# Performance work log

Hardware: AMD Instinct MI355X
Metric: run time of the kernel (lower is better)

Reference implementation:

```python
import jax, jax.numpy as jnp
import numpy as np

B, T, C = 2, 2048, 768
H = 12
D = C // H  # head size = 64
F = 4 * C
EPS = 1e-5


def _layernorm(x, g, b):
    mu = jnp.mean(x, axis=-1, keepdims=True)
    var = jnp.var(x, axis=-1, keepdims=True)
    return (x - mu) * jax.lax.rsqrt(var + EPS) * g + b


def setup_inputs() -> dict:
    key = jax.random.key(0)
    ks = jax.random.split(key, 16)
    s_in = 1.0 / np.sqrt(C)
    s_ff = 1.0 / np.sqrt(F)
    return {
        "x": jax.random.normal(ks[0], (B, T, C), dtype=jnp.float32),
        # per-head projection weights, stacked [H, C, D] (no bias, as in nn.Linear(bias=False))
        "Wq": jax.random.uniform(ks[1], (H, C, D), jnp.float32, -s_in, s_in),
        "Wk": jax.random.uniform(ks[2], (H, C, D), jnp.float32, -s_in, s_in),
        "Wv": jax.random.uniform(ks[3], (H, C, D), jnp.float32, -s_in, s_in),
        "Wp": jax.random.uniform(ks[4], (C, C), jnp.float32, -s_in, s_in),
        "bp": jax.random.uniform(ks[5], (C,), jnp.float32, -s_in, s_in),
        "W1": jax.random.uniform(ks[6], (C, F), jnp.float32, -s_in, s_in),
        "b1": jax.random.uniform(ks[7], (F,), jnp.float32, -s_in, s_in),
        "W2": jax.random.uniform(ks[8], (F, C), jnp.float32, -s_ff, s_ff),
        "b2": jax.random.uniform(ks[9], (C,), jnp.float32, -s_ff, s_ff),
        "ln1_g": jnp.ones((C,), jnp.float32),
        "ln1_b": jnp.zeros((C,), jnp.float32),
        "ln2_g": jnp.ones((C,), jnp.float32),
        "ln2_b": jnp.zeros((C,), jnp.float32),
    }


def reference(x, Wq, Wk, Wv, Wp, bp, W1, b1, W2, b2, ln1_g, ln1_b, ln2_g, ln2_b):
    # --- self-attention sublayer (pre-LN) ---
    h = _layernorm(x, ln1_g, ln1_b)                      # [B,T,C]
    q = jnp.einsum('btc,hcd->bhtd', h, Wq)
    k = jnp.einsum('btc,hcd->bhtd', h, Wk)
    v = jnp.einsum('btc,hcd->bhtd', h, Wv)
    # NOTE: original scales by C**-0.5 where C = n_embd (full width), not head size
    scale = C ** (-0.5)
    wei = jnp.einsum('bhtd,bhsd->bhts', q, k) * scale    # [B,H,T,T]
    causal = jnp.tril(jnp.ones((T, T), dtype=bool))
    wei = jnp.where(causal, wei, -jnp.inf)
    wei = jax.nn.softmax(wei, axis=-1)
    out = jnp.einsum('bhts,bhsd->bhtd', wei, v)          # [B,H,T,D]
    out = out.transpose(0, 2, 1, 3).reshape(B, T, C)     # concat heads
    sa = out @ Wp + bp
    x = x + sa
    # --- feed-forward sublayer (pre-LN); ReLU after BOTH linears, as in source ---
    h2 = _layernorm(x, ln2_g, ln2_b)
    ff = jax.nn.relu(jax.nn.relu(h2 @ W1 + b1) @ W2 + b2)
    return x + ff
```

## Files before the change

### kernel.cpp

```cpp
#include <hip/hip_runtime.h>
#include <hip/hip_bf16.h>

#define TSEQ 2048
#define CDIM 768
#define NHEAD 12
#define DHEAD 64
#define FDIM 3072
#define MROWS 4096
#define BH 24

typedef __attribute__((ext_vector_type(8))) short short8;
typedef __attribute__((ext_vector_type(4))) float f32x4;

__device__ inline unsigned short f2bf(float f) {
  __hip_bfloat16 h = __float2bfloat16(f);
  return __builtin_bit_cast(unsigned short, h);
}

__device__ inline void gload16(const unsigned short* g, unsigned short* l) {
  __builtin_amdgcn_global_load_lds(
      (const __attribute__((address_space(1))) unsigned int*)g,
      (__attribute__((address_space(3))) unsigned int*)l, 16, 0, 0);
}

__global__ __launch_bounds__(256) void prep_all(
    const float* __restrict__ Wq, const float* __restrict__ Wk,
    const float* __restrict__ Wv, const float* __restrict__ Wp,
    const float* __restrict__ W1, const float* __restrict__ W2,
    unsigned short* __restrict__ WqkvT, unsigned short* __restrict__ WpT,
    unsigned short* __restrict__ W1T, unsigned short* __restrict__ W2T,
    const float* __restrict__ x, const float* __restrict__ ln1g,
    const float* __restrict__ ln1b, unsigned short* __restrict__ h1) {
  __shared__ float tile[32][33];
  __shared__ float red[8];
  int b = blockIdx.x;
  if (b >= 6912) {
    int row = b - 6912;
    int tid = threadIdx.x;
    const float* xr = x + (size_t)row * CDIM;
    float v[3];
    float s = 0.f;
#pragma unroll
    for (int i = 0; i < 3; ++i) { v[i] = xr[tid + i * 256]; s += v[i]; }
#pragma unroll
    for (int m = 1; m < 64; m <<= 1) s += __shfl_xor(s, m);
    int w = tid >> 6;
    if ((tid & 63) == 0) red[w] = s;
    __syncthreads();
    float mean = (red[0] + red[1] + red[2] + red[3]) * (1.f / CDIM);
    float vs = 0.f;
#pragma unroll
    for (int i = 0; i < 3; ++i) { float d = v[i] - mean; vs += d * d; }
#pragma unroll
    for (int m = 1; m < 64; m <<= 1) vs += __shfl_xor(vs, m);
    if ((tid & 63) == 0) red[4 + w] = vs;
    __syncthreads();
    float var = (red[4] + red[5] + red[6] + red[7]) * (1.f / CDIM);
    float rstd = rsqrtf(var + 1e-5f);
    unsigned short* orow = h1 + (size_t)row * CDIM;
#pragma unroll
    for (int i = 0; i < 3; ++i) {
      int c = tid + i * 256;
      orow[c] = f2bf((v[i] - mean) * rstd * ln1g[c] + ln1b[c]);
    }
    return;
  }
  int xx = threadIdx.x & 31, y = threadIdx.x >> 5;
  if (b < 1728) {
    int cx = b % 24, dy = (b / 24) % 2, ph = b / 48;
    int proj = ph / NHEAD, h = ph % NHEAD;
    const float* in = (proj == 0 ? Wq : (proj == 1 ? Wk : Wv)) + (size_t)h * CDIM * DHEAD;
    int c0 = cx * 32, d0 = dy * 32;
#pragma unroll
    for (int i = 0; i < 4; ++i)
      tile[y + i * 8][xx] = in[(size_t)(c0 + y + i * 8) * DHEAD + d0 + xx];
    __syncthreads();
#pragma unroll
    for (int i = 0; i < 4; ++i)
      WqkvT[(size_t)(proj * CDIM + h * DHEAD + d0 + y + i * 8) * CDIM + c0 + xx] =
          f2bf(tile[xx][y + i * 8]);
  } else {
    const float* in;
    unsigned short* out;
    int R, C, bx, by;
    if (b < 2304) {
      int b2 = b - 1728;
      in = Wp; out = WpT; R = CDIM; C = CDIM; bx = b2 % 24; by = b2 / 24;
    } else if (b < 4608) {
      int b2 = b - 2304;
      in = W1; out = W1T; R = CDIM; C = FDIM; bx = b2 % 96; by = b2 / 96;
    } else {
      int b2 = b - 4608;
      in = W2; out = W2T; R = FDIM; C = CDIM; bx = b2 % 24; by = b2 / 24;
    }
    int c0 = bx * 32, r0 = by * 32;
#pragma unroll
    for (int i = 0; i < 4; ++i)
      tile[y + i * 8][xx] = in[(size_t)(r0 + y + i * 8) * C + c0 + xx];
    __syncthreads();
#pragma unroll
    for (int i = 0; i < 4; ++i)
      out[(size_t)(c0 + y + i * 8) * R + r0 + xx] = f2bf(tile[xx][y + i * 8]);
  }
}

__global__ __launch_bounds__(256) void ln_kernel(
    const float* __restrict__ x, const float* __restrict__ g,
    const float* __restrict__ b, unsigned short* __restrict__ out) {
  int row = blockIdx.x;
  int tid = threadIdx.x;
  const float* xr = x + (size_t)row * CDIM;
  float v[3];
  float s = 0.f;
#pragma unroll
  for (int i = 0; i < 3; ++i) { v[i] = xr[tid + i * 256]; s += v[i]; }
#pragma unroll
  for (int m = 1; m < 64; m <<= 1) s += __shfl_xor(s, m);
  __shared__ float red[8];
  int w = tid >> 6;
  if ((tid & 63) == 0) red[w] = s;
  __syncthreads();
  float mean = (red[0] + red[1] + red[2] + red[3]) * (1.f / CDIM);
  float vs = 0.f;
#pragma unroll
  for (int i = 0; i < 3; ++i) { float d = v[i] - mean; vs += d * d; }
#pragma unroll
  for (int m = 1; m < 64; m <<= 1) vs += __shfl_xor(vs, m);
  if ((tid & 63) == 0) red[4 + w] = vs;
  __syncthreads();
  float var = (red[4] + red[5] + red[6] + red[7]) * (1.f / CDIM);
  float rstd = rsqrtf(var + 1e-5f);
  unsigned short* orow = out + (size_t)row * CDIM;
#pragma unroll
  for (int i = 0; i < 3; ++i) {
    int c = tid + i * 256;
    orow[c] = f2bf((v[i] - mean) * rstd * g[c] + b[c]);
  }
}

template <int EPI>
__global__ __launch_bounds__(256) void gemm_bt(
    const unsigned short* __restrict__ A, const unsigned short* __restrict__ BT,
    int M, int N, int K,
    const float* __restrict__ bias, const float* __restrict__ aux,
    float* __restrict__ outf, unsigned short* __restrict__ outb,
    unsigned short* __restrict__ qo, unsigned short* __restrict__ ko,
    unsigned short* __restrict__ vo) {
  __shared__ unsigned short As[3][128 * 64];
  __shared__ unsigned short Bs[3][64 * 64];
  int tid = threadIdx.x;
  int lane = tid & 63, wave = tid >> 6;
  int l15 = lane & 15, lg = lane >> 4;
  int lr = lane >> 3, lc = lane & 7;
  size_t bm = (size_t)blockIdx.x * 128, bn = (size_t)blockIdx.y * 64;
  f32x4 acc[2][4] = {};
  int nk = K >> 6;

  auto stage = [&](int tk, int buf) {
    int kt = tk * 64;
#pragma unroll
    for (int i = 0; i < 4; ++i) {
      int r0 = (wave * 4 + i) * 8;
      gload16(A + (bm + r0 + lr) * K + kt + (lc ^ lr) * 8, &As[buf][r0 * 64]);
    }
#pragma unroll
    for (int i = 0; i < 2; ++i) {
      int r0 = (wave * 2 + i) * 8;
      gload16(BT + (bn + r0 + lr) * K + kt + (lc ^ lr) * 8, &Bs[buf][r0 * 64]);
    }
  };

  stage(0, 0);
  if (nk > 1) {
    stage(1, 1);
    asm volatile("s_waitcnt vmcnt(6)" ::: "memory");
  } else {
    asm volatile("s_waitcnt vmcnt(0)" ::: "memory");
  }
  __builtin_amdgcn_s_barrier();

  int cur = 0;
  for (int tk = 0; tk < nk; ++tk) {
    bool pre = (tk + 2 < nk);
    if (pre) stage(tk + 2, (cur + 2 >= 3) ? cur - 1 : cur + 2);
    __builtin_amdgcn_s_setprio(1);
#pragma unroll
    for (int kk = 0; kk < 64; kk += 32) {
      int kb = kk + lg * 8;
      short8 af[2], bfr[4];
#pragma unroll
      for (int m = 0; m < 2; ++m) {
        int row = wave * 32 + m * 16 + l15;
        af[m] = *reinterpret_cast<const short8*>(&As[cur][row * 64 + (kb ^ ((row & 7) << 3))]);
      }
#pragma unroll
      for (int n = 0; n < 4; ++n) {
        int row = n * 16 + l15;
        bfr[n] = *reinterpret_cast<const short8*>(&Bs[cur][row * 64 + (kb ^ ((row & 7) << 3))]);
      }
#pragma unroll
      for (int m = 0; m < 2; ++m)
#pragma unroll
        for (int n = 0; n < 4; ++n)
          acc[m][n] = __builtin_amdgcn_mfma_f32_16x16x32_bf16(af[m], bfr[n], acc[m][n], 0, 0, 0);
    }
    __builtin_amdgcn_s_setprio(0);
    if (pre) asm volatile("s_waitcnt vmcnt(6)" ::: "memory");
    else     asm volatile("s_waitcnt vmcnt(0)" ::: "memory");
    __builtin_amdgcn_s_barrier();
    cur = (cur == 2) ? 0 : cur + 1;
  }

#pragma unroll
  for (int m = 0; m < 2; ++m) {
#pragma unroll
    for (int n = 0; n < 4; ++n) {
#pragma unroll
      for (int r = 0; r < 4; ++r) {
        int row = (int)bm + wave * 32 + m * 16 + lg * 4 + r;
        int col = (int)bn + n * 16 + l15;
        float val = acc[m][n][r];
        if constexpr (EPI == 0) {
          int proj = col / CDIM, rem = col % CDIM;
          int h = rem >> 6, d = rem & 63;
          int b = row >> 11, t = row & (TSEQ - 1);
          if (proj == 0) {
            qo[(((size_t)(b * NHEAD + h)) * TSEQ + t) * DHEAD + d] =
                f2bf(val * 0.05205877247186126f);
          } else if (proj == 1) {
            ko[(((size_t)(b * NHEAD + h)) * TSEQ + t) * DHEAD + d] = f2bf(val);
          } else {
            vo[(((size_t)(b * NHEAD + h)) * DHEAD + d) * TSEQ + t] = f2bf(val);
          }
        } else if constexpr (EPI == 1) {
          size_t idx = (size_t)row * CDIM + col;
          outf[idx] = val + bias[col] + aux[idx];
        } else if constexpr (EPI == 2) {
          size_t idx = (size_t)row * FDIM + col;
          outb[idx] = f2bf(fmaxf(val + bias[col], 0.f));
        } else {
          size_t idx = (size_t)row * CDIM + col;
          outf[idx] = aux[idx] + fmaxf(val + bias[col], 0.f);
        }
      }
    }
  }
}

__global__ __launch_bounds__(256) void attn_kernel(
    const unsigned short* __restrict__ Q, const unsigned short* __restrict__ Kd,
    const unsigned short* __restrict__ VT, unsigned short* __restrict__ O) {
  __shared__ unsigned short Kl[3][64 * 64];
  __shared__ unsigned short Vl[3][64 * 64];
  __shared__ unsigned short plds[4][16 * 64];
  int tid = threadIdx.x;
  int wave = tid >> 6, lane = tid & 63;
  int l15 = lane & 15, lg = lane >> 4;
  int bid = blockIdx.x;
  int xcd = bid & 7, idx = bid >> 3;
  int bh = xcd * 3 + idx / 16;
  int p = idx & 15;
  const unsigned short* qp = Q + (size_t)bh * TSEQ * DHEAD;
  const unsigned short* kp = Kd + (size_t)bh * TSEQ * DHEAD;
  const unsigned short* vp = VT + (size_t)bh * DHEAD * TSEQ;
  unsigned short* pw = plds[wave];
  int b = bh / NHEAD, h = bh % NHEAD;

  short8 ones;
  {
    unsigned short ov = (l15 == 0) ? (unsigned short)0x3F80 : (unsigned short)0;
#pragma unroll
    for (int j = 0; j < 8; ++j) ones[j] = (short)ov;
  }

  int lr = lane >> 3, lc = lane & 7;
  int jsw = lc ^ lr;

  auto stage = [&](int t, int buf) {
    int s0 = t * 64;
#pragma unroll
    for (int i = 0; i < 2; ++i) {
      int r0 = (wave * 2 + i) * 8;
      gload16(kp + (size_t)(s0 + r0 + lr) * DHEAD + jsw * 8, &Kl[buf][r0 * 64]);
      gload16(vp + (size_t)(r0 + lr) * TSEQ + s0 + jsw * 8, &Vl[buf][r0 * 64]);
    }
  };

  auto run_stripe = [&](int stripe) {
    int qbase = stripe * 64 + wave * 16;
    int nt = stripe + 1;
    short8 qf[2];
#pragma unroll
    for (int kk = 0; kk < 2; ++kk)
      qf[kk] = *reinterpret_cast<const short8*>(
          qp + (size_t)(qbase + l15) * DHEAD + kk * 32 + lg * 8);
    f32x4 oacc[5] = {};

    stage(0, 0);
    if (nt > 1) {
      stage(1, 1);
      asm volatile("s_waitcnt vmcnt(4)" ::: "memory");
    } else {
      asm volatile("s_waitcnt vmcnt(0)" ::: "memory");
    }
    __builtin_amdgcn_s_barrier();

    for (int t = 0; t < nt; ++t) {
      int cur = t % 3;
      bool pre2 = (t + 2 < nt);
      if (pre2) stage(t + 2, (t + 2) % 3);
      int s0 = t * 64;
      f32x4 sacc[4] = {};
      __builtin_amdgcn_s_setprio(1);
#pragma unroll
      for (int st = 0; st < 4; ++st) {
        int row = st * 16 + l15;
        int sw = row & 7;
#pragma unroll
        for (int kk = 0; kk < 2; ++kk) {
          short8 kf = *reinterpret_cast<const short8*>(
              &Kl[cur][row * 64 + (((kk * 4 + lg) ^ sw) * 8)]);
          sacc[st] = __builtin_amdgcn_mfma_f32_16x16x32_bf16(qf[kk], kf, sacc[st], 0, 0, 0);
        }
      }
      __builtin_amdgcn_s_setprio(0);
      bool last = (t == nt - 1);
#pragma unroll
      for (int r = 0; r < 4; ++r) {
        int qrow = qbase + lg * 4 + r;
        int prow = lg * 4 + r;
        int psw = (prow & 7) << 3;
        if (last) {
#pragma unroll
          for (int st = 0; st < 4; ++st) {
            float pv = exp2f(sacc[st][r]);
            if (s0 + st * 16 + l15 > qrow) pv = 0.f;
            pw[prow * 64 + ((st * 16 + l15) ^ psw)] = f2bf(pv);
          }
        } else {
#pragma unroll
          for (int st = 0; st < 4; ++st)
            pw[prow * 64 + ((st * 16 + l15) ^ psw)] = f2bf(exp2f(sacc[st][r]));
        }
      }
      int prsw = (l15 & 7) << 3;
      short8 pa0 = *reinterpret_cast<const short8*>(&pw[l15 * 64 + ((lg * 8) ^ prsw)]);
      short8 pa1 = *reinterpret_cast<const short8*>(&pw[l15 * 64 + ((32 + lg * 8) ^ prsw)]);
      __builtin_amdgcn_s_setprio(1);
#pragma unroll
      for (int n = 0; n < 4; ++n) {
        int row = n * 16 + l15;
        int sw = row & 7;
        short8 vf0 = *reinterpret_cast<const short8*>(&Vl[cur][row * 64 + ((lg ^ sw) * 8)]);
        oacc[n] = __builtin_amdgcn_mfma_f32_16x16x32_bf16(pa0, vf0, oacc[n], 0, 0, 0);
        short8 vf1 = *reinterpret_cast<const short8*>(&Vl[cur][row * 64 + (((4 + lg) ^ sw) * 8)]);
        oacc[n] = __builtin_amdgcn_mfma_f32_16x16x32_bf16(pa1, vf1, oacc[n], 0, 0, 0);
      }
      oacc[4] = __builtin_amdgcn_mfma_f32_16x16x32_bf16(pa0, ones, oacc[4], 0, 0, 0);
      oacc[4] = __builtin_amdgcn_mfma_f32_16x16x32_bf16(pa1, ones, oacc[4], 0, 0, 0);
      __builtin_amdgcn_s_setprio(0);
      if (pre2) asm volatile("s_waitcnt vmcnt(4)" ::: "memory");
      else      asm volatile("s_waitcnt vmcnt(0)" ::: "memory");
      __builtin_amdgcn_s_barrier();
    }

#pragma unroll
    for (int r = 0; r < 4; ++r) {
      float lsum = __shfl(oacc[4][r], lane & 48);
      float inv = 1.f / lsum;
      int row = qbase + lg * 4 + r;
#pragma unroll
      for (int n = 0; n < 4; ++n)
        O[(size_t)(b * TSEQ + row) * CDIM + h * DHEAD + n * 16 + l15] =
            f2bf(oacc[n][r] * inv);
    }
  };

  run_stripe(31 - p);
  run_stripe(p);
}

extern "C" void kernel_launch(void* const* d_in, const int* in_sizes, int n_in,
                              void* d_out, int out_size, void* d_ws, size_t ws_size,
                              hipStream_t stream) {
  const float* x    = (const float*)d_in[0];
  const float* Wq   = (const float*)d_in[1];
  const float* Wk   = (const float*)d_in[2];
  const float* Wv   = (const float*)d_in[3];
  const float* Wp   = (const float*)d_in[4];
  const float* bp   = (const float*)d_in[5];
  const float* W1   = (const float*)d_in[6];
  const float* b1   = (const float*)d_in[7];
  const float* W2   = (const float*)d_in[8];
  const float* b2   = (const float*)d_in[9];
  const float* ln1g = (const float*)d_in[10];
  const float* ln1b = (const float*)d_in[11];
  const float* ln2g = (const float*)d_in[12];
  const float* ln2b = (const float*)d_in[13];
  float* out = (float*)d_out;

  char* ws = (char*)d_ws;
  auto alloc = [&](size_t bytes) {
    char* p = ws;
    ws += (bytes + 255) & ~(size_t)255;
    return p;
  };
  unsigned short* h1    = (unsigned short*)alloc((size_t)MROWS * CDIM * 2);
  unsigned short* WqkvT = (unsigned short*)alloc((size_t)3 * CDIM * CDIM * 2);
  unsigned short* WpT   = (unsigned short*)alloc((size_t)CDIM * CDIM * 2);
  unsigned short* W1T   = (unsigned short*)alloc((size_t)FDIM * CDIM * 2);
  unsigned short* W2T   = (unsigned short*)alloc((size_t)CDIM * FDIM * 2);
  unsigned short* Qb    = (unsigned short*)alloc((size_t)BH * TSEQ * DHEAD * 2);
  unsigned short* Kb    = (unsigned short*)alloc((size_t)BH * TSEQ * DHEAD * 2);
  unsigned short* VTb   = (unsigned short*)alloc((size_t)BH * TSEQ * DHEAD * 2);
  unsigned short* AO    = (unsigned short*)alloc((size_t)MROWS * CDIM * 2);
  float*          x1    = (float*)alloc((size_t)MROWS * CDIM * 4);
  unsigned short* h2    = (unsigned short*)alloc((size_t)MROWS * CDIM * 2);
  unsigned short* a1    = (unsigned short*)alloc((size_t)MROWS * FDIM * 2);

  prep_all<<<11008, 256, 0, stream>>>(Wq, Wk, Wv, Wp, W1, W2,
                                      WqkvT, WpT, W1T, W2T, x, ln1g, ln1b, h1);
  gemm_bt<0><<<dim3(32, 36), 256, 0, stream>>>(h1, WqkvT, MROWS, 3 * CDIM, CDIM,
                                               nullptr, nullptr, nullptr, nullptr, Qb, Kb, VTb);
  attn_kernel<<<384, 256, 0, stream>>>(Qb, Kb, VTb, AO);
  gemm_bt<1><<<dim3(32, 12), 256, 0, stream>>>(AO, WpT, MROWS, CDIM, CDIM,
                                               bp, x, x1, nullptr, nullptr, nullptr, nullptr);
  ln_kernel<<<4096, 256, 0, stream>>>(x1, ln2g, ln2b, h2);
  gemm_bt<2><<<dim3(32, 48), 256, 0, stream>>>(h2, W1T, MROWS, FDIM, CDIM,
                                               b1, nullptr, nullptr, a1, nullptr, nullptr, nullptr);
  gemm_bt<3><<<dim3(32, 12), 256, 0, stream>>>(a1, W2T, MROWS, CDIM, FDIM,
                                               b2, x1, out, nullptr, nullptr, nullptr, nullptr);
}
```

Measured before the change: 197.2 us.

## Use 128x128 GEMM tiles with XCD-aware block remap, drop triple buffering

The GEMM tile grows from 128x64 to 128x128, with each wave computing a 64x64 sub-tile to raise MFMA work per LDS load. Launches become 1D grids, and block IDs are remapped so consecutive logical tiles land on the same XCD chiplet, which should improve L2 reuse. The three-stage async prefetch pipeline is replaced by a single-buffered load/sync/compute loop. This removes global-to-LDS overlap and halves the block count, so the small N=768 GEMMs (192 blocks) may underfill the GPU.

```diff
diff --git a/kernel.cpp b/kernel.cpp
--- a/kernel.cpp
+++ b/kernel.cpp
@@ -146,79 +146,60 @@
     float* __restrict__ outf, unsigned short* __restrict__ outb,
     unsigned short* __restrict__ qo, unsigned short* __restrict__ ko,
     unsigned short* __restrict__ vo) {
-  __shared__ unsigned short As[3][128 * 64];
-  __shared__ unsigned short Bs[3][64 * 64];
+  __shared__ unsigned short As[128 * 64];
+  __shared__ unsigned short Bs[128 * 64];
   int tid = threadIdx.x;
   int lane = tid & 63, wave = tid >> 6;
+  int wr = wave >> 1, wc = wave & 1;
   int l15 = lane & 15, lg = lane >> 4;
   int lr = lane >> 3, lc = lane & 7;
-  size_t bm = (size_t)blockIdx.x * 128, bn = (size_t)blockIdx.y * 64;
-  f32x4 acc[2][4] = {};
-  int nk = K >> 6;
-
-  auto stage = [&](int tk, int buf) {
-    int kt = tk * 64;
+  int chunk = gridDim.x >> 3;
+  int logical = (blockIdx.x & 7) * chunk + (blockIdx.x >> 3);
+  int mt = M >> 7;
+  size_t bm = (size_t)(logical % mt) * 128, bn = (size_t)(logical / mt) * 128;
+  f32x4 acc[4][4] = {};
+
+  for (int kt = 0; kt < K; kt += 64) {
 #pragma unroll
     for (int i = 0; i < 4; ++i) {
       int r0 = (wave * 4 + i) * 8;
-      gload16(A + (bm + r0 + lr) * K + kt + (lc ^ lr) * 8, &As[buf][r0 * 64]);
-    }
-#pragma unroll
-    for (int i = 0; i < 2; ++i) {
-      int r0 = (wave * 2 + i) * 8;
-      gload16(BT + (bn + r0 + lr) * K + kt + (lc ^ lr) * 8, &Bs[buf][r0 * 64]);
-    }
-  };
-
-  stage(0, 0);
-  if (nk > 1) {
-    stage(1, 1);
-    asm volatile("s_waitcnt vmcnt(6)" ::: "memory");
-  } else {
-    asm volatile("s_waitcnt vmcnt(0)" ::: "memory");
-  }
-  __builtin_amdgcn_s_barrier();
-
-  int cur = 0;
-  for (int tk = 0; tk < nk; ++tk) {
-    bool pre = (tk + 2 < nk);
-    if (pre) stage(tk + 2, (cur + 2 >= 3) ? cur - 1 : cur + 2);
+      gload16(A + (bm + r0 + lr) * K + kt + (lc ^ lr) * 8, &As[r0 * 64]);
+      gload16(BT + (bn + r0 + lr) * K + kt + (lc ^ lr) * 8, &Bs[r0 * 64]);
+    }
+    __syncthreads();
     __builtin_amdgcn_s_setprio(1);
 #pragma unroll
     for (int kk = 0; kk < 64; kk += 32) {
       int kb = kk + lg * 8;
-      short8 af[2], bfr[4];
-#pragma unroll
-      for (int m = 0; m < 2; ++m) {
-        int row = wave * 32 + m * 16 + l15;
-        af[m] = *reinterpret_cast<const short8*>(&As[cur][row * 64 + (kb ^ ((row & 7) << 3))]);
+      short8 af[4], bfr[4];
+#pragma unroll
+      for (int m = 0; m < 4; ++m) {
+        int row = wr * 64 + m * 16 + l15;
+        af[m] = *reinterpret_cast<const short8*>(&As[row * 64 + (kb ^ ((row & 7) << 3))]);
       }
 #pragma unroll
       for (int n = 0; n < 4; ++n) {
-        int row = n * 16 + l15;
-        bfr[n] = *reinterpret_cast<const short8*>(&Bs[cur][row * 64 + (kb ^ ((row & 7) << 3))]);
-      }
-#pragma unroll
-      for (int m = 0; m < 2; ++m)
+        int row = wc * 64 + n * 16 + l15;
+        bfr[n] = *reinterpret_cast<const short8*>(&Bs[row * 64 + (kb ^ ((row & 7) << 3))]);
+      }
+#pragma unroll
+      for (int m = 0; m < 4; ++m)
 #pragma unroll
         for (int n = 0; n < 4; ++n)
           acc[m][n] = __builtin_amdgcn_mfma_f32_16x16x32_bf16(af[m], bfr[n], acc[m][n], 0, 0, 0);
     }
     __builtin_amdgcn_s_setprio(0);
-    if (pre) asm volatile("s_waitcnt vmcnt(6)" ::: "memory");
-    else     asm volatile("s_waitcnt vmcnt(0)" ::: "memory");
-    __builtin_amdgcn_s_barrier();
-    cur = (cur == 2) ? 0 : cur + 1;
-  }
-
-#pragma unroll
-  for (int m = 0; m < 2; ++m) {
+    __syncthreads();
+  }
+
+#pragma unroll
+  for (int m = 0; m < 4; ++m) {
 #pragma unroll
     for (int n = 0; n < 4; ++n) {
 #pragma unroll
       for (int r = 0; r < 4; ++r) {
-        int row = (int)bm + wave * 32 + m * 16 + lg * 4 + r;
-        int col = (int)bn + n * 16 + l15;
+        int row = (int)bm + wr * 64 + m * 16 + lg * 4 + r;
+        int col = (int)bn + wc * 64 + n * 16 + l15;
         float val = acc[m][n][r];
         if constexpr (EPI == 0) {
           int proj = col / CDIM, rem = col % CDIM;
@@ -420,14 +401,14 @@
 
   prep_all<<<11008, 256, 0, stream>>>(Wq, Wk, Wv, Wp, W1, W2,
                                       WqkvT, WpT, W1T, W2T, x, ln1g, ln1b, h1);
-  gemm_bt<0><<<dim3(32, 36), 256, 0, stream>>>(h1, WqkvT, MROWS, 3 * CDIM, CDIM,
-                                               nullptr, nullptr, nullptr, nullptr, Qb, Kb, VTb);
+  gemm_bt<0><<<576, 256, 0, stream>>>(h1, WqkvT, MROWS, 3 * CDIM, CDIM,
+                                      nullptr, nullptr, nullptr, nullptr, Qb, Kb, VTb);
   attn_kernel<<<384, 256, 0, stream>>>(Qb, Kb, VTb, AO);
-  gemm_bt<1><<<dim3(32, 12), 256, 0, stream>>>(AO, WpT, MROWS, CDIM, CDIM,
-                                               bp, x, x1, nullptr, nullptr, nullptr, nullptr);
+  gemm_bt<1><<<192, 256, 0, stream>>>(AO, WpT, MROWS, CDIM, CDIM,
+                                      bp, x, x1, nullptr, nullptr, nullptr, nullptr);
   ln_kernel<<<4096, 256, 0, stream>>>(x1, ln2g, ln2b, h2);
-  gemm_bt<2><<<dim3(32, 48), 256, 0, stream>>>(h2, W1T, MROWS, FDIM, CDIM,
-                                               b1, nullptr, nullptr, a1, nullptr, nullptr, nullptr);
-  gemm_bt<3><<<dim3(32, 12), 256, 0, stream>>>(a1, W2T, MROWS, CDIM, FDIM,
-                                               b2, x1, out, nullptr, nullptr, nullptr, nullptr);
-}
+  gemm_bt<2><<<768, 256, 0, stream>>>(h2, W1T, MROWS, FDIM, CDIM,
+                                      b1, nullptr, nullptr, a1, nullptr, nullptr, nullptr);
+  gemm_bt<3><<<192, 256, 0, stream>>>(a1, W2T, MROWS, CDIM, FDIM,
+                                      b2, x1, out, nullptr, nullptr, nullptr, nullptr);
+}
```

Result: slower. 213.4 us (+8.3%).
